# Optimization experiments

Measured on AMD Instinct MI355X. Metric: run time of the kernel, lower is better.

The kernel has to match this reference:

```python
import jax, jax.numpy as jnp
import numpy as np

B, D, L = 4096, 128, 4
ALPHA = 1.0
SLOPE = 0.1  # LeakyReLU negative slope


def _leaky(h):
    return jnp.where(h > 0, h, SLOPE * h)


def _dleaky(h):
    return jnp.where(h > 0, 1.0, SLOPE).astype(h.dtype)


def setup_inputs() -> dict:
    key = jax.random.key(0)
    ks = jax.random.split(key, 7)
    scale = 0.5 / np.sqrt(D)  # keep residual roughly Lipschitz < 1
    x = jax.random.normal(ks[0], (B, D), jnp.float32)
    W1 = jax.random.normal(ks[1], (L, D, D), jnp.float32) * scale
    b1 = jax.random.normal(ks[2], (L, D), jnp.float32) * 0.01
    W2 = jax.random.normal(ks[3], (L, D, D), jnp.float32) * scale
    b2 = jax.random.normal(ks[4], (L, D), jnp.float32) * 0.01
    W3 = jax.random.normal(ks[5], (L, D, D), jnp.float32) * scale
    b3 = jax.random.normal(ks[6], (L, D), jnp.float32) * 0.01
    return {"x": x, "W1": W1, "b1": b1, "W2": W2, "b2": b2, "W3": W3, "b3": b3}


def reference(x, W1, b1, W2, b2, W3, b3):
    logdet = jnp.zeros(x.shape[0], x.dtype)
    for i in range(L):  # small fixed number of structurally distinct blocks
        w1, w2, w3 = W1[i], W2[i], W3[i]
        # --- block forward: x <- x + alpha * f(x) ---
        h1 = x @ w1.T + b1[i]
        h2 = _leaky(h1) @ w2.T + b2[i]
        f = _leaky(h2) @ w3.T + b3[i]
        x = x + ALPHA * f
        # --- log|det J_f| evaluated at the NEW x (as in the original code) ---
        g1 = x @ w1.T + b1[i]          # [B, D] pre-activation 1
        d1 = _dleaky(g1)
        g2 = _leaky(g1) @ w2.T + b2[i]  # [B, D] pre-activation 2
        d2 = _dleaky(g2)
        # J[b] = w3 @ diag(d2[b]) @ w2 @ diag(d1[b]) @ w1  -> [B, D, D]
        J = (w3[None, :, :] * d2[:, None, :]) @ w2
        J = (J * d1[:, None, :]) @ w1
        s = jnp.linalg.svd(J, compute_uv=False)  # [B, D] singular values
        logdet = logdet + jnp.sum(jnp.log(s), axis=-1)
    return x, logdet
```

## Files before the change

### kernel.cpp

```cpp
#include <hip/hip_runtime.h>

typedef __attribute__((ext_vector_type(8))) short short8;
typedef __attribute__((ext_vector_type(4))) float float4f;

#define PITCH 136
#define ROWS 32
#define LOG_SLOPE -2.302585092994046f
#define LN2 0.6931471805599453f
#define NBLK 140
#define LDS_BYTES 69760
#define WS_BIAS 4160
#define WS_WPLANES 8192
#define NWELEM 196608

__device__ __forceinline__ float bf2f(unsigned int u) {
    return __builtin_bit_cast(float, u << 16);
}
__device__ __forceinline__ unsigned short f2bf(float f) {
    unsigned int x = __builtin_bit_cast(unsigned int, f);
    x += 0x7fff + ((x >> 16) & 1);
    return (unsigned short)(x >> 16);
}
__device__ __forceinline__ float4f vmsub(float4f a, float s, float4f b) {
    a[0] -= s * b[0]; a[1] -= s * b[1]; a[2] -= s * b[2]; a[3] -= s * b[3];
    return a;
}
__device__ __forceinline__ float4f vscale(float4f a, float s) {
    a[0] *= s; a[1] *= s; a[2] *= s; a[3] *= s;
    return a;
}

template<int ISF32>
__device__ __forceinline__ float ldv(const void* p, int i) {
    if (ISF32) return ((const float*)p)[i];
    return bf2f(((const unsigned short*)p)[i]);
}

__device__ __forceinline__ int detect_f32(const unsigned short* W1u, int lane) {
    unsigned int u = W1u[lane * 2];
    unsigned int e = (u >> 7) & 0xFF;
    int bad = (e < 64) || (e > 135);
    return __ballot(bad) != 0ull;
}

__device__ __forceinline__ float4f mfma16(short8 a, short8 b, float4f c) {
    return __builtin_amdgcn_mfma_f32_16x16x32_bf16(a, b, c, 0, 0, 0);
}

__device__ __forceinline__ void split8(float4f a, float4f b, short8& hi, short8& lo) {
#pragma unroll
    for (int j = 0; j < 4; ++j) {
        float v = a[j]; unsigned short h = f2bf(v);
        hi[j] = (short)h; lo[j] = (short)f2bf(v - bf2f(h));
        v = b[j]; h = f2bf(v);
        hi[4 + j] = (short)h; lo[4 + j] = (short)f2bf(v - bf2f(h));
    }
}

__global__ void k_prep(const void* __restrict__ W1, const void* __restrict__ W2,
                       const void* __restrict__ W3, const void* __restrict__ b1,
                       const void* __restrict__ b2, const void* __restrict__ b3,
                       float* __restrict__ ws) {
    const int tid = threadIdx.x, bid = blockIdx.x;
    const int isf32 = detect_f32((const unsigned short*)W1, tid & 63);
    unsigned short* whi = (unsigned short*)(ws + WS_WPLANES);
    unsigned short* wlo = whi + NWELEM;
    if (bid < 96) {
        int s = (bid * 256 + tid) * 8;
        int mat = s >> 14, off = s & 16383;
        int wsel = mat >> 2;
        const void* Wm = wsel == 0 ? W1 : (wsel == 1 ? W2 : W3);
        int src = (mat & 3) * 16384 + off;
        short8 hi, lo;
        if (isf32) {
            const float* p = (const float*)Wm + src;
            split8(*(const float4f*)p, *(const float4f*)(p + 4), hi, lo);
        } else {
            hi = *(const short8*)((const unsigned short*)Wm + src);
            lo = (short8){0, 0, 0, 0, 0, 0, 0, 0};
        }
        *(short8*)(whi + s) = hi;
        *(short8*)(wlo + s) = lo;
    } else {
        for (int e = tid; e < 1536; e += 256) {
            int bsel = e >> 9, idx = e & 511;
            const void* bp = bsel == 0 ? b1 : (bsel == 1 ? b2 : b3);
            ws[WS_BIAS + e] = isf32 ? ((const float*)bp)[idx]
                                    : bf2f(((const unsigned short*)bp)[idx]);
        }
        if (tid == 0) ((int*)ws)[0] = 0;
    }
}

struct W8 { short8 v[16]; };

__device__ __forceinline__ W8 loadW(const unsigned short* __restrict__ wh,
                                    const unsigned short* __restrict__ wl,
                                    int c0, int c1, int q) {
    W8 r;
#pragma unroll
    for (int kk = 0; kk < 4; ++kk) {
        const int kc = kk * 32 + q * 8;
        r.v[kk * 4 + 0] = *(const short8*)(wh + c0 * 128 + kc);
        r.v[kk * 4 + 1] = *(const short8*)(wh + c1 * 128 + kc);
        r.v[kk * 4 + 2] = *(const short8*)(wl + c0 * 128 + kc);
        r.v[kk * 4 + 3] = *(const short8*)(wl + c1 * 128 + kc);
    }
    return r;
}

template<int MODE>
__device__ __forceinline__ W8 matvec(const W8& w,
        const unsigned short* inh, const unsigned short* inl,
        unsigned short* outh, unsigned short* outl,
        const unsigned short* resh, const unsigned short* resl,
        const unsigned short* __restrict__ nwh, const unsigned short* __restrict__ nwl,
        const float* __restrict__ bias,
        int lane, int colb, int* cnt) {
    const int m = lane & 15, q = lane >> 4;
    const int c0 = colb + m, c1 = colb + 16 + m;
    float b0 = bias[c0], b1v = bias[c1];
    float4f acc[2][2];
#pragma unroll
    for (int rt = 0; rt < 2; ++rt) {
        acc[rt][0] = (float4f){b0, b0, b0, b0};
        acc[rt][1] = (float4f){b1v, b1v, b1v, b1v};
    }
    __syncthreads();
    W8 wn = loadW(nwh, nwl, c0, c1, q);
#pragma unroll
    for (int kk = 0; kk < 4; ++kk) {
        const int kc = kk * 32 + q * 8;
#pragma unroll
        for (int rt = 0; rt < 2; ++rt) {
            short8 xh = *(const short8*)(inh + (rt * 16 + m) * PITCH + kc);
            short8 xl = *(const short8*)(inl + (rt * 16 + m) * PITCH + kc);
            acc[rt][0] = mfma16(xh, w.v[kk * 4 + 0], acc[rt][0]);
            acc[rt][0] = mfma16(xl, w.v[kk * 4 + 0], acc[rt][0]);
            acc[rt][0] = mfma16(xh, w.v[kk * 4 + 2], acc[rt][0]);
            acc[rt][1] = mfma16(xh, w.v[kk * 4 + 1], acc[rt][1]);
            acc[rt][1] = mfma16(xl, w.v[kk * 4 + 1], acc[rt][1]);
            acc[rt][1] = mfma16(xh, w.v[kk * 4 + 3], acc[rt][1]);
        }
    }
    int c[2][4];
#pragma unroll
    for (int rt = 0; rt < 2; ++rt) {
#pragma unroll
        for (int r = 0; r < 4; ++r) {
            float v0 = acc[rt][0][r], v1 = acc[rt][1][r];
            int row = rt * 16 + q * 4 + r;
            int o0 = row * PITCH + c0, o1 = row * PITCH + c1;
            if (MODE == 1) {
                v0 += bf2f(resh[o0]) + bf2f(resl[o0]);
                v1 += bf2f(resh[o1]) + bf2f(resl[o1]);
            }
            if (MODE >= 2) c[rt][r] = (v0 <= 0.0f) + (v1 <= 0.0f);
            if (MODE == 0 || MODE == 2) {
                v0 = v0 > 0.0f ? v0 : 0.1f * v0;
                v1 = v1 > 0.0f ? v1 : 0.1f * v1;
            }
            if (MODE != 3) {
                unsigned short h0 = f2bf(v0);
                outh[o0] = h0; outl[o0] = f2bf(v0 - bf2f(h0));
                unsigned short h1 = f2bf(v1);
                outh[o1] = h1; outl[o1] = f2bf(v1 - bf2f(h1));
            }
        }
    }
    if (MODE >= 2) {
#pragma unroll
        for (int rt = 0; rt < 2; ++rt) {
#pragma unroll
            for (int r = 0; r < 4; ++r) {
                int cc = c[rt][r];
                cc += __shfl_xor(cc, 1);
                cc += __shfl_xor(cc, 2);
                cc += __shfl_xor(cc, 4);
                cc += __shfl_xor(cc, 8);
                if (m == 0) atomicAdd(&cnt[rt * 16 + q * 4 + r], cc);
            }
        }
    }
    return wn;
}

template<int ISF32>
__device__ __forceinline__ void fwd(int bid, int tid, int lane, char* ldsb,
                                    const void* x, const float* ws, void* out,
                                    float* wsw) {
    unsigned short* P = (unsigned short*)ldsb;
    unsigned short* Ah = P;
    unsigned short* Al = P + 1 * ROWS * PITCH;
    unsigned short* Bh = P + 2 * ROWS * PITCH;
    unsigned short* Bl = P + 3 * ROWS * PITCH;
    unsigned short* Th = P + 4 * ROWS * PITCH;
    unsigned short* Tl = P + 5 * ROWS * PITCH;
    unsigned short* Uh = P + 6 * ROWS * PITCH;
    unsigned short* Ul = P + 7 * ROWS * PITCH;
    int* cnt = (int*)(P + 8 * ROWS * PITCH);
    const unsigned short* whi = (const unsigned short*)(ws + WS_WPLANES);
    const unsigned short* wlo = whi + NWELEM;
    const float* bias = ws + WS_BIAS;
    const int r0 = bid * ROWS;
    const int m = lane & 15, q = lane >> 4;
    const int colb = (tid >> 6) * 32;
    const int c0 = colb + m, c1 = colb + 16 + m;
    W8 wcur = loadW(whi, wlo, c0, c1, q);
    for (int e = tid; e < ROWS * 128; e += 256) {
        int r = e >> 7, c = e & 127;
        float v = ldv<ISF32>(x, (r0 + r) * 128 + c);
        unsigned short h = f2bf(v);
        Ah[r * PITCH + c] = h;
        Al[r * PITCH + c] = f2bf(v - bf2f(h));
    }
    if (tid < ROWS) cnt[tid] = 0;
    unsigned short *curh = Ah, *curl = Al, *othh = Bh, *othl = Bl;
#pragma unroll 1
    for (int layer = 0; layer < 4; ++layer) {
        const unsigned short* w1h = whi + (0 + layer) * 16384;
        const unsigned short* w1l = wlo + (0 + layer) * 16384;
        const unsigned short* w2h = whi + (4 + layer) * 16384;
        const unsigned short* w2l = wlo + (4 + layer) * 16384;
        const unsigned short* w3h = whi + (8 + layer) * 16384;
        const unsigned short* w3l = wlo + (8 + layer) * 16384;
        const unsigned short* n1h = whi + ((layer + 1) & 3) * 16384;
        const unsigned short* n1l = wlo + ((layer + 1) & 3) * 16384;
        const float* b1p = bias + layer * 128;
        const float* b2p = bias + 512 + layer * 128;
        const float* b3p = bias + 1024 + layer * 128;
        wcur = matvec<0>(wcur, curh, curl, Th, Tl, 0, 0, w2h, w2l, b1p, lane, colb, cnt);
        wcur = matvec<0>(wcur, Th, Tl, Uh, Ul, 0, 0, w3h, w3l, b2p, lane, colb, cnt);
        wcur = matvec<1>(wcur, Uh, Ul, othh, othl, curh, curl, w1h, w1l, b3p, lane, colb, cnt);
        wcur = matvec<2>(wcur, othh, othl, Th, Tl, 0, 0, w2h, w2l, b1p, lane, colb, cnt);
        wcur = matvec<3>(wcur, Th, Tl, Th, Tl, 0, 0, n1h, n1l, b2p, lane, colb, cnt);
        unsigned short* t;
        t = curh; curh = othh; othh = t;
        t = curl; curl = othl; othl = t;
    }
    __syncthreads();
    for (int e = tid; e < ROWS * 128; e += 256) {
        int r = e >> 7, c = e & 127;
        float v = bf2f(curh[r * PITCH + c]) + bf2f(curl[r * PITCH + c]);
        if (ISF32) ((float*)out)[(r0 + r) * 128 + c] = v;
        else ((unsigned short*)out)[(r0 + r) * 128 + c] = f2bf(v);
    }
    if (tid < ROWS) wsw[64 + r0 + tid] = (float)cnt[tid];
}

template<int ISF32>
__device__ __forceinline__ float lu_logdet(int id, int tid, float* lds,
        const void* W1, const void* W2, const void* W3) {
    const int wsel = id % 3;
    const void* Wm = (wsel == 0 ? W1 : (wsel == 1 ? W2 : W3));
    const int ofs = (id / 3) * 16384;
    const int tx = tid & 31, ty = tid >> 5;
    float* rowbuf = lds;
    float* colbuf = lds + 1024;
    float4f V[16];
#pragma unroll
    for (int m = 0; m < 16; ++m) {
        int base = ofs + (ty + 8 * m) * 128 + 4 * tx;
        if (ISF32) {
            V[m] = *(const float4f*)((const float*)Wm + base);
        } else {
            ushort4 u = *(const ushort4*)((const unsigned short*)Wm + base);
            V[m] = (float4f){bf2f(u.x), bf2f(u.y), bf2f(u.z), bf2f(u.w)};
        }
    }
    if (ty < 4) *(float4f*)&rowbuf[ty * 128 + 4 * tx] = V[0];
    if (tx == 0) {
#pragma unroll
        for (int j = 0; j < 4; ++j) {
#pragma unroll
            for (int mg = 0; mg < 4; ++mg) {
                float4f t = {V[mg * 4 + 0][j], V[mg * 4 + 1][j],
                             V[mg * 4 + 2][j], V[mg * 4 + 3][j]};
                *(float4f*)&colbuf[j * 128 + ty * 16 + mg * 4] = t;
            }
        }
    }
    __syncthreads();
    float logacc = 0.0f;
#pragma unroll 1
    for (int kap = 0; kap < 32; ++kap) {
        const int K = kap * 4;
        const int buf = (kap & 1) * 512;
        float4f D[4], R[4], C[4][4];
#pragma unroll
        for (int j = 0; j < 4; ++j) {
            D[j] = *(const float4f*)&rowbuf[buf + j * 128 + K];
            R[j] = *(const float4f*)&rowbuf[buf + j * 128 + 4 * tx];
#pragma unroll
            for (int mg = 0; mg < 4; ++mg)
                C[j][mg] = *(const float4f*)&colbuf[buf + j * 128 + ty * 16 + mg * 4];
        }
        float p0 = D[0][0], i0 = 1.0f / p0;
        float l10 = D[1][0] * i0, l20 = D[2][0] * i0, l30 = D[3][0] * i0;
        D[1] = vmsub(D[1], l10, D[0]); R[1] = vmsub(R[1], l10, R[0]);
        D[2] = vmsub(D[2], l20, D[0]); R[2] = vmsub(R[2], l20, R[0]);
        D[3] = vmsub(D[3], l30, D[0]); R[3] = vmsub(R[3], l30, R[0]);
        float p1 = D[1][1], i1 = 1.0f / p1;
        float l21 = D[2][1] * i1, l31 = D[3][1] * i1;
        D[2] = vmsub(D[2], l21, D[1]); R[2] = vmsub(R[2], l21, R[1]);
        D[3] = vmsub(D[3], l31, D[1]); R[3] = vmsub(R[3], l31, R[1]);
        float p2 = D[2][2], i2 = 1.0f / p2;
        float l32 = D[3][2] * i2;
        D[3] = vmsub(D[3], l32, D[2]); R[3] = vmsub(R[3], l32, R[2]);
        float p3 = D[3][3], i3 = 1.0f / p3;
        logacc += __log2f(fabsf(p0)) + __log2f(fabsf(p1))
                + __log2f(fabsf(p2)) + __log2f(fabsf(p3));
        float4f X3 = vscale(R[3], i3);
        float4f X2 = vscale(vmsub(R[2], D[2][3], X3), i2);
        float4f X1 = vscale(vmsub(vmsub(R[1], D[1][2], X2), D[1][3], X3), i1);
        float4f X0 = vscale(vmsub(vmsub(vmsub(R[0], D[0][1], X1),
                                        D[0][2], X2), D[0][3], X3), i0);
#pragma unroll
        for (int mg = 0; mg < 4; ++mg) {
#pragma unroll
            for (int e = 0; e < 4; ++e) {
                float4f v = V[mg * 4 + e];
                v = vmsub(v, C[0][mg][e], X0);
                v = vmsub(v, C[1][mg][e], X1);
                v = vmsub(v, C[2][mg][e], X2);
                v = vmsub(v, C[3][mg][e], X3);
                V[mg * 4 + e] = v;
            }
        }
        if (kap < 31) {
            const int nbuf = ((kap + 1) & 1) * 512;
            const int tb = (kap & 1) ? 0 : 4;
            const int mn = (kap + 1) >> 1;
            if (ty >= tb && ty < tb + 4) {
                float4f val;
                switch (mn) {
                case 0:  val = V[0];  break; case 1:  val = V[1];  break;
                case 2:  val = V[2];  break; case 3:  val = V[3];  break;
                case 4:  val = V[4];  break; case 5:  val = V[5];  break;
                case 6:  val = V[6];  break; case 7:  val = V[7];  break;
                case 8:  val = V[8];  break; case 9:  val = V[9];  break;
                case 10: val = V[10]; break; case 11: val = V[11]; break;
                case 12: val = V[12]; break; case 13: val = V[13]; break;
                case 14: val = V[14]; break; default: val = V[15]; break;
                }
                *(float4f*)&rowbuf[nbuf + (ty - tb) * 128 + 4 * tx] = val;
            }
            if (tx == kap + 1) {
#pragma unroll
                for (int j = 0; j < 4; ++j) {
#pragma unroll
                    for (int mg = 0; mg < 4; ++mg) {
                        float4f t = {V[mg * 4 + 0][j], V[mg * 4 + 1][j],
                                     V[mg * 4 + 2][j], V[mg * 4 + 3][j]};
                        *(float4f*)&colbuf[nbuf + j * 128 + ty * 16 + mg * 4] = t;
                    }
                }
            }
        }
        __syncthreads();
    }
    return logacc * LN2;
}

__global__ __launch_bounds__(256) void k_main(
        const void* __restrict__ x,
        const void* __restrict__ W1, const void* __restrict__ b1,
        const void* __restrict__ W2, const void* __restrict__ b2,
        const void* __restrict__ W3, const void* __restrict__ b3,
        void* __restrict__ out, float* __restrict__ ws) {
    extern __shared__ __align__(16) char ldsb[];
    __shared__ int s_last;
    const int tid = threadIdx.x;
    const int lane = tid & 63;
    const int isf32 = detect_f32((const unsigned short*)W1, lane);

    if (blockIdx.x < 12) {
        float ld = isf32 ? lu_logdet<1>(blockIdx.x, tid, (float*)ldsb, W1, W2, W3)
                         : lu_logdet<0>(blockIdx.x, tid, (float*)ldsb, W1, W2, W3);
        if (tid == 0) ws[2 + blockIdx.x] = ld;
    } else {
        const int bid = blockIdx.x - 12;
        if (isf32) fwd<1>(bid, tid, lane, ldsb, x, ws, out, ws);
        else       fwd<0>(bid, tid, lane, ldsb, x, ws, out, ws);
    }

    __threadfence();
    if (tid == 0) s_last = (atomicAdd((int*)ws, 1) == NBLK - 1);
    __syncthreads();
    if (!s_last) return;
    __threadfence();
    float s = 0.0f;
#pragma unroll
    for (int i = 0; i < 12; ++i) s += ws[2 + i];
    for (int b = tid; b < 4096; b += 256) {
        float v = s + LOG_SLOPE * ws[64 + b];
        if (isf32) ((float*)out)[524288 + b] = v;
        else ((unsigned short*)out)[524288 + b] = f2bf(v);
    }
}

extern "C" void kernel_launch(void* const* d_in, const int* in_sizes, int n_in,
                              void* d_out, int out_size, void* d_ws, size_t ws_size,
                              hipStream_t stream) {
    const void* x  = d_in[0];
    const void* W1 = d_in[1];
    const void* b1 = d_in[2];
    const void* W2 = d_in[3];
    const void* b2 = d_in[4];
    const void* W3 = d_in[5];
    const void* b3 = d_in[6];
    float* ws = (float*)d_ws;

    hipLaunchKernelGGL(k_prep, dim3(97), dim3(256), 0, stream,
                       W1, W2, W3, b1, b2, b3, ws);
    hipLaunchKernelGGL(k_main, dim3(NBLK), dim3(256), LDS_BYTES, stream,
                       x, W1, b1, W2, b2, W3, b3, d_out, ws);
}
```

Before: 134.7 us.

## Use 1024-thread blocks with 64-row tiles split across 16 waves

The forward path now uses 64 rows per block and 16 waves. Each wave computes a 16-row by 32-column tile instead of two 16-row tiles, which halves the serial MFMA chain per wave and puts more waves on each CU to hide LDS and weight-load latency. The grid shrinks from 140 to 76 blocks, and the LU logdet blocks drop their extra threads early. In exchange, fewer CUs are used, every wave still loads the full weight fragments, so weight traffic per row doubles, and the 1024-thread launch bound caps registers, which risks spills in the LU path.

Result: slower. 357.0 us (+165.0%).

```diff
diff --git a/kernel.cpp b/kernel.cpp
--- a/kernel.cpp
+++ b/kernel.cpp
@@ -4,11 +4,11 @@
 typedef __attribute__((ext_vector_type(4))) float float4f;
 
 #define PITCH 136
-#define ROWS 32
+#define ROWS 64
 #define LOG_SLOPE -2.302585092994046f
 #define LN2 0.6931471805599453f
-#define NBLK 140
-#define LDS_BYTES 69760
+#define NBLK 76
+#define LDS_BYTES 139520
 #define WS_BIAS 4160
 #define WS_WPLANES 8192
 #define NWELEM 196608
@@ -116,70 +116,57 @@
         const unsigned short* resh, const unsigned short* resl,
         const unsigned short* __restrict__ nwh, const unsigned short* __restrict__ nwl,
         const float* __restrict__ bias,
-        int lane, int colb, int* cnt) {
+        int lane, int colb, int rb, int* cnt) {
     const int m = lane & 15, q = lane >> 4;
     const int c0 = colb + m, c1 = colb + 16 + m;
     float b0 = bias[c0], b1v = bias[c1];
-    float4f acc[2][2];
-#pragma unroll
-    for (int rt = 0; rt < 2; ++rt) {
-        acc[rt][0] = (float4f){b0, b0, b0, b0};
-        acc[rt][1] = (float4f){b1v, b1v, b1v, b1v};
-    }
+    float4f acc0 = (float4f){b0, b0, b0, b0};
+    float4f acc1 = (float4f){b1v, b1v, b1v, b1v};
     __syncthreads();
     W8 wn = loadW(nwh, nwl, c0, c1, q);
 #pragma unroll
     for (int kk = 0; kk < 4; ++kk) {
         const int kc = kk * 32 + q * 8;
-#pragma unroll
-        for (int rt = 0; rt < 2; ++rt) {
-            short8 xh = *(const short8*)(inh + (rt * 16 + m) * PITCH + kc);
-            short8 xl = *(const short8*)(inl + (rt * 16 + m) * PITCH + kc);
-            acc[rt][0] = mfma16(xh, w.v[kk * 4 + 0], acc[rt][0]);
-            acc[rt][0] = mfma16(xl, w.v[kk * 4 + 0], acc[rt][0]);
-            acc[rt][0] = mfma16(xh, w.v[kk * 4 + 2], acc[rt][0]);
-            acc[rt][1] = mfma16(xh, w.v[kk * 4 + 1], acc[rt][1]);
-            acc[rt][1] = mfma16(xl, w.v[kk * 4 + 1], acc[rt][1]);
-            acc[rt][1] = mfma16(xh, w.v[kk * 4 + 3], acc[rt][1]);
-        }
-    }
-    int c[2][4];
-#pragma unroll
-    for (int rt = 0; rt < 2; ++rt) {
+        short8 xh = *(const short8*)(inh + (rb + m) * PITCH + kc);
+        short8 xl = *(const short8*)(inl + (rb + m) * PITCH + kc);
+        acc0 = mfma16(xh, w.v[kk * 4 + 0], acc0);
+        acc0 = mfma16(xl, w.v[kk * 4 + 0], acc0);
+        acc0 = mfma16(xh, w.v[kk * 4 + 2], acc0);
+        acc1 = mfma16(xh, w.v[kk * 4 + 1], acc1);
+        acc1 = mfma16(xl, w.v[kk * 4 + 1], acc1);
+        acc1 = mfma16(xh, w.v[kk * 4 + 3], acc1);
+    }
+    int c[4];
+#pragma unroll
+    for (int r = 0; r < 4; ++r) {
+        float v0 = acc0[r], v1 = acc1[r];
+        int row = rb + q * 4 + r;
+        int o0 = row * PITCH + c0, o1 = row * PITCH + c1;
+        if (MODE == 1) {
+            v0 += bf2f(resh[o0]) + bf2f(resl[o0]);
+            v1 += bf2f(resh[o1]) + bf2f(resl[o1]);
+        }
+        if (MODE >= 2) c[r] = (v0 <= 0.0f) + (v1 <= 0.0f);
+        if (MODE == 0 || MODE == 2) {
+            v0 = v0 > 0.0f ? v0 : 0.1f * v0;
+            v1 = v1 > 0.0f ? v1 : 0.1f * v1;
+        }
+        if (MODE != 3) {
+            unsigned short h0 = f2bf(v0);
+            outh[o0] = h0; outl[o0] = f2bf(v0 - bf2f(h0));
+            unsigned short h1 = f2bf(v1);
+            outh[o1] = h1; outl[o1] = f2bf(v1 - bf2f(h1));
+        }
+    }
+    if (MODE >= 2) {
 #pragma unroll
         for (int r = 0; r < 4; ++r) {
-            float v0 = acc[rt][0][r], v1 = acc[rt][1][r];
-            int row = rt * 16 + q * 4 + r;
-            int o0 = row * PITCH + c0, o1 = row * PITCH + c1;
-            if (MODE == 1) {
-                v0 += bf2f(resh[o0]) + bf2f(resl[o0]);
-                v1 += bf2f(resh[o1]) + bf2f(resl[o1]);
-            }
-            if (MODE >= 2) c[rt][r] = (v0 <= 0.0f) + (v1 <= 0.0f);
-            if (MODE == 0 || MODE == 2) {
-                v0 = v0 > 0.0f ? v0 : 0.1f * v0;
-                v1 = v1 > 0.0f ? v1 : 0.1f * v1;
-            }
-            if (MODE != 3) {
-                unsigned short h0 = f2bf(v0);
-                outh[o0] = h0; outl[o0] = f2bf(v0 - bf2f(h0));
-                unsigned short h1 = f2bf(v1);
-                outh[o1] = h1; outl[o1] = f2bf(v1 - bf2f(h1));
-            }
-        }
-    }
-    if (MODE >= 2) {
-#pragma unroll
-        for (int rt = 0; rt < 2; ++rt) {
-#pragma unroll
-            for (int r = 0; r < 4; ++r) {
-                int cc = c[rt][r];
-                cc += __shfl_xor(cc, 1);
-                cc += __shfl_xor(cc, 2);
-                cc += __shfl_xor(cc, 4);
-                cc += __shfl_xor(cc, 8);
-                if (m == 0) atomicAdd(&cnt[rt * 16 + q * 4 + r], cc);
-            }
+            int cc = c[r];
+            cc += __shfl_xor(cc, 1);
+            cc += __shfl_xor(cc, 2);
+            cc += __shfl_xor(cc, 4);
+            cc += __shfl_xor(cc, 8);
+            if (m == 0) atomicAdd(&cnt[rb + q * 4 + r], cc);
         }
     }
     return wn;
@@ -204,10 +191,12 @@
     const float* bias = ws + WS_BIAS;
     const int r0 = bid * ROWS;
     const int m = lane & 15, q = lane >> 4;
-    const int colb = (tid >> 6) * 32;
+    const int wv = tid >> 6;
+    const int colb = (wv & 3) * 32;
+    const int rb = (wv >> 2) * 16;
     const int c0 = colb + m, c1 = colb + 16 + m;
     W8 wcur = loadW(whi, wlo, c0, c1, q);
-    for (int e = tid; e < ROWS * 128; e += 256) {
+    for (int e = tid; e < ROWS * 128; e += 1024) {
         int r = e >> 7, c = e & 127;
         float v = ldv<ISF32>(x, (r0 + r) * 128 + c);
         unsigned short h = f2bf(v);
@@ -229,17 +218,17 @@
         const float* b1p = bias + layer * 128;
         const float* b2p = bias + 512 + layer * 128;
         const float* b3p = bias + 1024 + layer * 128;
-        wcur = matvec<0>(wcur, curh, curl, Th, Tl, 0, 0, w2h, w2l, b1p, lane, colb, cnt);
-        wcur = matvec<0>(wcur, Th, Tl, Uh, Ul, 0, 0, w3h, w3l, b2p, lane, colb, cnt);
-        wcur = matvec<1>(wcur, Uh, Ul, othh, othl, curh, curl, w1h, w1l, b3p, lane, colb, cnt);
-        wcur = matvec<2>(wcur, othh, othl, Th, Tl, 0, 0, w2h, w2l, b1p, lane, colb, cnt);
-        wcur = matvec<3>(wcur, Th, Tl, Th, Tl, 0, 0, n1h, n1l, b2p, lane, colb, cnt);
+        wcur = matvec<0>(wcur, curh, curl, Th, Tl, 0, 0, w2h, w2l, b1p, lane, colb, rb, cnt);
+        wcur = matvec<0>(wcur, Th, Tl, Uh, Ul, 0, 0, w3h, w3l, b2p, lane, colb, rb, cnt);
+        wcur = matvec<1>(wcur, Uh, Ul, othh, othl, curh, curl, w1h, w1l, b3p, lane, colb, rb, cnt);
+        wcur = matvec<2>(wcur, othh, othl, Th, Tl, 0, 0, w2h, w2l, b1p, lane, colb, rb, cnt);
+        wcur = matvec<3>(wcur, Th, Tl, Th, Tl, 0, 0, n1h, n1l, b2p, lane, colb, rb, cnt);
         unsigned short* t;
         t = curh; curh = othh; othh = t;
         t = curl; curl = othl; othl = t;
     }
     __syncthreads();
-    for (int e = tid; e < ROWS * 128; e += 256) {
+    for (int e = tid; e < ROWS * 128; e += 1024) {
         int r = e >> 7, c = e & 127;
         float v = bf2f(curh[r * PITCH + c]) + bf2f(curl[r * PITCH + c]);
         if (ISF32) ((float*)out)[(r0 + r) * 128 + c] = v;
@@ -362,7 +351,7 @@
     return logacc * LN2;
 }
 
-__global__ __launch_bounds__(256) void k_main(
+__global__ __launch_bounds__(1024) void k_main(
         const void* __restrict__ x,
         const void* __restrict__ W1, const void* __restrict__ b1,
         const void* __restrict__ W2, const void* __restrict__ b2,
@@ -372,6 +361,7 @@
     __shared__ int s_last;
     const int tid = threadIdx.x;
     const int lane = tid & 63;
+    if (blockIdx.x < 12 && tid >= 256) return;
     const int isf32 = detect_f32((const unsigned short*)W1, lane);
 
     if (blockIdx.x < 12) {
@@ -389,13 +379,15 @@
     __syncthreads();
     if (!s_last) return;
     __threadfence();
-    float s = 0.0f;
-#pragma unroll
-    for (int i = 0; i < 12; ++i) s += ws[2 + i];
-    for (int b = tid; b < 4096; b += 256) {
-        float v = s + LOG_SLOPE * ws[64 + b];
-        if (isf32) ((float*)out)[524288 + b] = v;
-        else ((unsigned short*)out)[524288 + b] = f2bf(v);
+    if (tid < 256) {
+        float s = 0.0f;
+#pragma unroll
+        for (int i = 0; i < 12; ++i) s += ws[2 + i];
+        for (int b = tid; b < 4096; b += 256) {
+            float v = s + LOG_SLOPE * ws[64 + b];
+            if (isf32) ((float*)out)[524288 + b] = v;
+            else ((unsigned short*)out)[524288 + b] = f2bf(v);
+        }
     }
 }
 
@@ -413,6 +405,6 @@
 
     hipLaunchKernelGGL(k_prep, dim3(97), dim3(256), 0, stream,
                        W1, W2, W3, b1, b2, b3, ws);
-    hipLaunchKernelGGL(k_main, dim3(NBLK), dim3(256), LDS_BYTES, stream,
+    hipLaunchKernelGGL(k_main, dim3(NBLK), dim3(1024), LDS_BYTES, stream,
                        x, W1, b1, W2, b2, W3, b3, d_out, ws);
 }
```

## Software-pipeline forward and logdet matvecs across layers to pair independent GEMMs

Applied to the files above, without the earlier changes.

Restructures the per-block layer loop so each layer's logdet-side matvecs (W2 and W3 on the new x) run paired with the next layer's forward matvecs (W2 and W3 on the next hidden state), interleaving their MFMAs. This cuts the number of barrier-separated matvec stages per layer from five to three and gives the MFMA pipe two independent accumulator chains. The cost is doubled weight registers (two prefetched weight sets), which is why launch bounds now pin one block per SM. Register pressure or spills are the main risk.

New measurement: 140.3 us. 4.1% more time.

```diff
diff --git a/kernel.cpp b/kernel.cpp
--- a/kernel.cpp
+++ b/kernel.cpp
@@ -93,6 +93,7 @@
 }
 
 struct W8 { short8 v[16]; };
+struct W8x2 { W8 a, b; };
 
 __device__ __forceinline__ W8 loadW(const unsigned short* __restrict__ wh,
                                     const unsigned short* __restrict__ wl,
@@ -109,12 +110,13 @@
     return r;
 }
 
-template<int MODE>
-__device__ __forceinline__ W8 matvec(const W8& w,
+template<int MODE, int NPREF>
+__device__ __forceinline__ W8x2 matvecS(const W8& w,
         const unsigned short* inh, const unsigned short* inl,
         unsigned short* outh, unsigned short* outl,
         const unsigned short* resh, const unsigned short* resl,
-        const unsigned short* __restrict__ nwh, const unsigned short* __restrict__ nwl,
+        const unsigned short* __restrict__ nah, const unsigned short* __restrict__ nal,
+        const unsigned short* __restrict__ nbh, const unsigned short* __restrict__ nbl,
         const float* __restrict__ bias,
         int lane, int colb, int* cnt) {
     const int m = lane & 15, q = lane >> 4;
@@ -127,7 +129,9 @@
         acc[rt][1] = (float4f){b1v, b1v, b1v, b1v};
     }
     __syncthreads();
-    W8 wn = loadW(nwh, nwl, c0, c1, q);
+    W8x2 wn;
+    wn.a = loadW(nah, nal, c0, c1, q);
+    if constexpr (NPREF == 2) wn.b = loadW(nbh, nbl, c0, c1, q);
 #pragma unroll
     for (int kk = 0; kk < 4; ++kk) {
         const int kc = kk * 32 + q * 8;
@@ -180,6 +184,96 @@
                 cc += __shfl_xor(cc, 8);
                 if (m == 0) atomicAdd(&cnt[rt * 16 + q * 4 + r], cc);
             }
+        }
+    }
+    return wn;
+}
+
+template<int MODEB, int NPREF>
+__device__ __forceinline__ W8x2 matvecP(const W8x2& w,
+        const unsigned short* inAh, const unsigned short* inAl,
+        const unsigned short* inBh, const unsigned short* inBl,
+        unsigned short* outAh, unsigned short* outAl,
+        unsigned short* outBh, unsigned short* outBl,
+        const unsigned short* __restrict__ nah, const unsigned short* __restrict__ nal,
+        const unsigned short* __restrict__ nbh, const unsigned short* __restrict__ nbl,
+        const float* __restrict__ biasA, const float* __restrict__ biasB,
+        int lane, int colb, int* cnt) {
+    const int m = lane & 15, q = lane >> 4;
+    const int c0 = colb + m, c1 = colb + 16 + m;
+    float bA0 = biasA[c0], bA1 = biasA[c1];
+    float bB0 = biasB[c0], bB1 = biasB[c1];
+    float4f aA[2][2], aB[2][2];
+#pragma unroll
+    for (int rt = 0; rt < 2; ++rt) {
+        aA[rt][0] = (float4f){bA0, bA0, bA0, bA0};
+        aA[rt][1] = (float4f){bA1, bA1, bA1, bA1};
+        aB[rt][0] = (float4f){bB0, bB0, bB0, bB0};
+        aB[rt][1] = (float4f){bB1, bB1, bB1, bB1};
+    }
+    __syncthreads();
+    W8x2 wn;
+    wn.a = loadW(nah, nal, c0, c1, q);
+    if constexpr (NPREF == 2) wn.b = loadW(nbh, nbl, c0, c1, q);
+#pragma unroll
+    for (int kk = 0; kk < 4; ++kk) {
+        const int kc = kk * 32 + q * 8;
+#pragma unroll
+        for (int rt = 0; rt < 2; ++rt) {
+            short8 xah = *(const short8*)(inAh + (rt * 16 + m) * PITCH + kc);
+            short8 xal = *(const short8*)(inAl + (rt * 16 + m) * PITCH + kc);
+            short8 xbh = *(const short8*)(inBh + (rt * 16 + m) * PITCH + kc);
+            short8 xbl = *(const short8*)(inBl + (rt * 16 + m) * PITCH + kc);
+            aA[rt][0] = mfma16(xah, w.a.v[kk * 4 + 0], aA[rt][0]);
+            aB[rt][0] = mfma16(xbh, w.b.v[kk * 4 + 0], aB[rt][0]);
+            aA[rt][0] = mfma16(xal, w.a.v[kk * 4 + 0], aA[rt][0]);
+            aB[rt][0] = mfma16(xbl, w.b.v[kk * 4 + 0], aB[rt][0]);
+            aA[rt][0] = mfma16(xah, w.a.v[kk * 4 + 2], aA[rt][0]);
+            aB[rt][0] = mfma16(xbh, w.b.v[kk * 4 + 2], aB[rt][0]);
+            aA[rt][1] = mfma16(xah, w.a.v[kk * 4 + 1], aA[rt][1]);
+            aB[rt][1] = mfma16(xbh, w.b.v[kk * 4 + 1], aB[rt][1]);
+            aA[rt][1] = mfma16(xal, w.a.v[kk * 4 + 1], aA[rt][1]);
+            aB[rt][1] = mfma16(xbl, w.b.v[kk * 4 + 1], aB[rt][1]);
+            aA[rt][1] = mfma16(xah, w.a.v[kk * 4 + 3], aA[rt][1]);
+            aB[rt][1] = mfma16(xbh, w.b.v[kk * 4 + 3], aB[rt][1]);
+        }
+    }
+    int c[2][4];
+#pragma unroll
+    for (int rt = 0; rt < 2; ++rt) {
+#pragma unroll
+        for (int r = 0; r < 4; ++r) {
+            int row = rt * 16 + q * 4 + r;
+            int o0 = row * PITCH + c0, o1 = row * PITCH + c1;
+            float vA0 = aA[rt][0][r], vA1 = aA[rt][1][r];
+            vA0 = vA0 > 0.0f ? vA0 : 0.1f * vA0;
+            vA1 = vA1 > 0.0f ? vA1 : 0.1f * vA1;
+            unsigned short hA0 = f2bf(vA0);
+            outAh[o0] = hA0; outAl[o0] = f2bf(vA0 - bf2f(hA0));
+            unsigned short hA1 = f2bf(vA1);
+            outAh[o1] = hA1; outAl[o1] = f2bf(vA1 - bf2f(hA1));
+            float vB0 = aB[rt][0][r], vB1 = aB[rt][1][r];
+            c[rt][r] = (vB0 <= 0.0f) + (vB1 <= 0.0f);
+            if (MODEB == 2) {
+                vB0 = vB0 > 0.0f ? vB0 : 0.1f * vB0;
+                vB1 = vB1 > 0.0f ? vB1 : 0.1f * vB1;
+                unsigned short hB0 = f2bf(vB0);
+                outBh[o0] = hB0; outBl[o0] = f2bf(vB0 - bf2f(hB0));
+                unsigned short hB1 = f2bf(vB1);
+                outBh[o1] = hB1; outBl[o1] = f2bf(vB1 - bf2f(hB1));
+            }
+        }
+    }
+#pragma unroll
+    for (int rt = 0; rt < 2; ++rt) {
+#pragma unroll
+        for (int r = 0; r < 4; ++r) {
+            int cc = c[rt][r];
+            cc += __shfl_xor(cc, 1);
+            cc += __shfl_xor(cc, 2);
+            cc += __shfl_xor(cc, 4);
+            cc += __shfl_xor(cc, 8);
+            if (m == 0) atomicAdd(&cnt[rt * 16 + q * 4 + r], cc);
         }
     }
     return wn;
@@ -206,7 +300,7 @@
     const int m = lane & 15, q = lane >> 4;
     const int colb = (tid >> 6) * 32;
     const int c0 = colb + m, c1 = colb + 16 + m;
-    W8 wcur = loadW(whi, wlo, c0, c1, q);
+    W8 w10 = loadW(whi, wlo, c0, c1, q);
     for (int e = tid; e < ROWS * 128; e += 256) {
         int r = e >> 7, c = e & 127;
         float v = ldv<ISF32>(x, (r0 + r) * 128 + c);
@@ -215,33 +309,55 @@
         Al[r * PITCH + c] = f2bf(v - bf2f(h));
     }
     if (tid < ROWS) cnt[tid] = 0;
-    unsigned short *curh = Ah, *curl = Al, *othh = Bh, *othl = Bl;
+
+    W8x2 wc;
+    wc = matvecS<0, 1>(w10, Ah, Al, Th, Tl, 0, 0,
+                       whi + 4 * 16384, wlo + 4 * 16384, 0, 0,
+                       bias, lane, colb, cnt);
+    wc = matvecS<0, 1>(wc.a, Th, Tl, Uh, Ul, 0, 0,
+                       whi + 8 * 16384, wlo + 8 * 16384, 0, 0,
+                       bias + 512, lane, colb, cnt);
+    wc = matvecS<1, 2>(wc.a, Uh, Ul, Bh, Bl, Ah, Al,
+                       whi + 1 * 16384, wlo + 1 * 16384,
+                       whi + 0 * 16384, wlo + 0 * 16384,
+                       bias + 1024, lane, colb, cnt);
+    unsigned short *xnh = Bh, *xnl = Bl, *ddh = Ah, *ddl = Al;
 #pragma unroll 1
-    for (int layer = 0; layer < 4; ++layer) {
-        const unsigned short* w1h = whi + (0 + layer) * 16384;
-        const unsigned short* w1l = wlo + (0 + layer) * 16384;
-        const unsigned short* w2h = whi + (4 + layer) * 16384;
-        const unsigned short* w2l = wlo + (4 + layer) * 16384;
-        const unsigned short* w3h = whi + (8 + layer) * 16384;
-        const unsigned short* w3l = wlo + (8 + layer) * 16384;
-        const unsigned short* n1h = whi + ((layer + 1) & 3) * 16384;
-        const unsigned short* n1l = wlo + ((layer + 1) & 3) * 16384;
-        const float* b1p = bias + layer * 128;
-        const float* b2p = bias + 512 + layer * 128;
-        const float* b3p = bias + 1024 + layer * 128;
-        wcur = matvec<0>(wcur, curh, curl, Th, Tl, 0, 0, w2h, w2l, b1p, lane, colb, cnt);
-        wcur = matvec<0>(wcur, Th, Tl, Uh, Ul, 0, 0, w3h, w3l, b2p, lane, colb, cnt);
-        wcur = matvec<1>(wcur, Uh, Ul, othh, othl, curh, curl, w1h, w1l, b3p, lane, colb, cnt);
-        wcur = matvec<2>(wcur, othh, othl, Th, Tl, 0, 0, w2h, w2l, b1p, lane, colb, cnt);
-        wcur = matvec<3>(wcur, Th, Tl, Th, Tl, 0, 0, n1h, n1l, b2p, lane, colb, cnt);
+    for (int L = 0; L < 3; ++L) {
+        const int Ln = L + 1, Lnn = (L < 2) ? L + 2 : 3;
+        const unsigned short* w2nh = whi + (4 + Ln) * 16384;
+        const unsigned short* w2nl = wlo + (4 + Ln) * 16384;
+        const unsigned short* w2ch = whi + (4 + L) * 16384;
+        const unsigned short* w2cl = wlo + (4 + L) * 16384;
+        const unsigned short* w3nh = whi + (8 + Ln) * 16384;
+        const unsigned short* w3nl = wlo + (8 + Ln) * 16384;
+        const unsigned short* w1ah = whi + Lnn * 16384;
+        const unsigned short* w1al = wlo + Lnn * 16384;
+        const unsigned short* w1bh = whi + Ln * 16384;
+        const unsigned short* w1bl = wlo + Ln * 16384;
+        wc = matvecP<2, 2>(wc, xnh, xnl, xnh, xnl, Th, Tl, ddh, ddl,
+                           w2nh, w2nl, w2ch, w2cl,
+                           bias + Ln * 128, bias + L * 128, lane, colb, cnt);
+        wc = matvecP<3, 1>(wc, Th, Tl, ddh, ddl, Uh, Ul, Th, Tl,
+                           w3nh, w3nl, 0, 0,
+                           bias + 512 + Ln * 128, bias + 512 + L * 128, lane, colb, cnt);
+        wc = matvecS<1, 2>(wc.a, Uh, Ul, ddh, ddl, xnh, xnl,
+                           w1ah, w1al, w1bh, w1bl,
+                           bias + 1024 + Ln * 128, lane, colb, cnt);
         unsigned short* t;
-        t = curh; curh = othh; othh = t;
-        t = curl; curl = othl; othl = t;
-    }
+        t = xnh; xnh = ddh; ddh = t;
+        t = xnl; xnl = ddl; ddl = t;
+    }
+    wc = matvecS<2, 1>(wc.a, xnh, xnl, Th, Tl, 0, 0,
+                       whi + 7 * 16384, wlo + 7 * 16384, 0, 0,
+                       bias + 3 * 128, lane, colb, cnt);
+    matvecS<3, 1>(wc.a, Th, Tl, Th, Tl, 0, 0,
+                  whi + 7 * 16384, wlo + 7 * 16384, 0, 0,
+                  bias + 512 + 3 * 128, lane, colb, cnt);
     __syncthreads();
     for (int e = tid; e < ROWS * 128; e += 256) {
         int r = e >> 7, c = e & 127;
-        float v = bf2f(curh[r * PITCH + c]) + bf2f(curl[r * PITCH + c]);
+        float v = bf2f(xnh[r * PITCH + c]) + bf2f(xnl[r * PITCH + c]);
         if (ISF32) ((float*)out)[(r0 + r) * 128 + c] = v;
         else ((unsigned short*)out)[(r0 + r) * 128 + c] = f2bf(v);
     }
@@ -362,7 +478,7 @@
     return logacc * LN2;
 }
 
-__global__ __launch_bounds__(256) void k_main(
+__global__ __launch_bounds__(256, 1) void k_main(
         const void* __restrict__ x,
         const void* __restrict__ W1, const void* __restrict__ b1,
         const void* __restrict__ W2, const void* __restrict__ b2,
```

## Keep per-layer weight fragments in registers and reuse across forward and Jacobian passes

Applied to the files above, without the earlier changes.

Within each layer the W1 and W2 register fragments are now held in separate register sets (wA, wB, wC) and reused for the second evaluation at the new x, so they are no longer reloaded from global memory. This removes two of the five weight fragment loads per layer. The barrier is replaced by an inline s_waitcnt lgkmcnt(0) plus s_barrier so pending global loads are not waited on at each sync, and launch bounds are set to one block per SIMD budget so more registers are available. The cost is much higher register pressure from three live 16-short8 weight sets, which risks spilling.

Result: faster. 128.8 us (-4.4%).

```diff
diff --git a/kernel.cpp b/kernel.cpp
--- a/kernel.cpp
+++ b/kernel.cpp
@@ -28,6 +28,10 @@
 __device__ __forceinline__ float4f vscale(float4f a, float s) {
     a[0] *= s; a[1] *= s; a[2] *= s; a[3] *= s;
     return a;
+}
+
+__device__ __forceinline__ void bar_lgkm() {
+    asm volatile("s_waitcnt lgkmcnt(0)\n\ts_barrier" ::: "memory");
 }
 
 template<int ISF32>
@@ -109,7 +113,7 @@
     return r;
 }
 
-template<int MODE>
+template<int MODE, int DOLOAD>
 __device__ __forceinline__ W8 matvec(const W8& w,
         const unsigned short* inh, const unsigned short* inl,
         unsigned short* outh, unsigned short* outl,
@@ -126,8 +130,11 @@
         acc[rt][0] = (float4f){b0, b0, b0, b0};
         acc[rt][1] = (float4f){b1v, b1v, b1v, b1v};
     }
-    __syncthreads();
-    W8 wn = loadW(nwh, nwl, c0, c1, q);
+    bar_lgkm();
+    W8 wn;
+    if constexpr (DOLOAD) {
+        wn = loadW(nwh, nwl, c0, c1, q);
+    }
 #pragma unroll
     for (int kk = 0; kk < 4; ++kk) {
         const int kc = kk * 32 + q * 8;
@@ -182,7 +189,8 @@
             }
         }
     }
-    return wn;
+    if constexpr (DOLOAD) return wn;
+    else return w;
 }
 
 template<int ISF32>
@@ -206,7 +214,8 @@
     const int m = lane & 15, q = lane >> 4;
     const int colb = (tid >> 6) * 32;
     const int c0 = colb + m, c1 = colb + 16 + m;
-    W8 wcur = loadW(whi, wlo, c0, c1, q);
+    W8 wA = loadW(whi, wlo, c0, c1, q);
+    W8 wB, wC;
     for (int e = tid; e < ROWS * 128; e += 256) {
         int r = e >> 7, c = e & 127;
         float v = ldv<ISF32>(x, (r0 + r) * 128 + c);
@@ -218,8 +227,6 @@
     unsigned short *curh = Ah, *curl = Al, *othh = Bh, *othl = Bl;
 #pragma unroll 1
     for (int layer = 0; layer < 4; ++layer) {
-        const unsigned short* w1h = whi + (0 + layer) * 16384;
-        const unsigned short* w1l = wlo + (0 + layer) * 16384;
         const unsigned short* w2h = whi + (4 + layer) * 16384;
         const unsigned short* w2l = wlo + (4 + layer) * 16384;
         const unsigned short* w3h = whi + (8 + layer) * 16384;
@@ -229,16 +236,16 @@
         const float* b1p = bias + layer * 128;
         const float* b2p = bias + 512 + layer * 128;
         const float* b3p = bias + 1024 + layer * 128;
-        wcur = matvec<0>(wcur, curh, curl, Th, Tl, 0, 0, w2h, w2l, b1p, lane, colb, cnt);
-        wcur = matvec<0>(wcur, Th, Tl, Uh, Ul, 0, 0, w3h, w3l, b2p, lane, colb, cnt);
-        wcur = matvec<1>(wcur, Uh, Ul, othh, othl, curh, curl, w1h, w1l, b3p, lane, colb, cnt);
-        wcur = matvec<2>(wcur, othh, othl, Th, Tl, 0, 0, w2h, w2l, b1p, lane, colb, cnt);
-        wcur = matvec<3>(wcur, Th, Tl, Th, Tl, 0, 0, n1h, n1l, b2p, lane, colb, cnt);
+        wB = matvec<0, 1>(wA, curh, curl, Th, Tl, 0, 0, w2h, w2l, b1p, lane, colb, cnt);
+        wC = matvec<0, 1>(wB, Th, Tl, Uh, Ul, 0, 0, w3h, w3l, b2p, lane, colb, cnt);
+        matvec<1, 0>(wC, Uh, Ul, othh, othl, curh, curl, 0, 0, b3p, lane, colb, cnt);
+        matvec<2, 0>(wA, othh, othl, Th, Tl, 0, 0, 0, 0, b1p, lane, colb, cnt);
+        wA = matvec<3, 1>(wB, Th, Tl, Th, Tl, 0, 0, n1h, n1l, b2p, lane, colb, cnt);
         unsigned short* t;
         t = curh; curh = othh; othh = t;
         t = curl; curl = othl; othl = t;
     }
-    __syncthreads();
+    bar_lgkm();
     for (int e = tid; e < ROWS * 128; e += 256) {
         int r = e >> 7, c = e & 127;
         float v = bf2f(curh[r * PITCH + c]) + bf2f(curl[r * PITCH + c]);
@@ -362,7 +369,7 @@
     return logacc * LN2;
 }
 
-__global__ __launch_bounds__(256) void k_main(
+__global__ __launch_bounds__(256, 1) void k_main(
         const void* __restrict__ x,
         const void* __restrict__ W1, const void* __restrict__ b1,
         const void* __restrict__ W2, const void* __restrict__ b2,
```
